# Kernel optimization log

Measured on AMD Instinct MI355X. Metric: run time of the kernel, lower is better.

Reference implementation:

```python
import jax, jax.numpy as jnp
import numpy as np

N_CLASSES = 2
LAMBD = 0.5
BATCH = 16777216  # 2**24


def _cost_matrix(n):
    # M[i, j] = (j - i)**2 for j > i, else 0 (upper-triangular squared distance)
    i = jnp.arange(n)[:, None]
    j = jnp.arange(n)[None, :]
    return jnp.where(j > i, (j - i).astype(jnp.float32) ** 2, 0.0)


def setup_inputs() -> dict:
    key = jax.random.key(0)
    k1, k2 = jax.random.split(key)
    outputs = jax.random.normal(k1, (BATCH, N_CLASSES), dtype=jnp.float32)
    labels = jax.random.randint(k2, (BATCH,), 0, N_CLASSES, dtype=jnp.int64)
    return {"outputs": outputs, "labels": labels}


def reference(outputs, labels):
    n = N_CLASSES
    M = _cost_matrix(n)

    # criterion: cross-entropy with mean reduction
    logp = jax.nn.log_softmax(outputs, axis=-1)           # [B, C]
    ce = -jnp.mean(jnp.take_along_axis(logp, labels[:, None], axis=1))

    # prediction = argmax over classes (torch.max(outputs, 1)[1])
    prediction = jnp.argmax(outputs, axis=1)              # [B]

    # CS = M[prediction, labels] : gather of cost weights
    CS = M[prediction, labels]                            # [B]

    # confusion matrix via single scatter-add histogram: cm[t, p] += 1
    flat_idx = labels * n + prediction
    cm = jax.ops.segment_sum(jnp.ones_like(flat_idx, dtype=jnp.float32),
                             flat_idx, num_segments=n * n)
    TP = cm[1 * n + 1]
    TN = cm[0 * n + 0]
    FP = cm[0 * n + 1]
    FN = cm[1 * n + 0]

    nonzero = (TP > 0) & (TN > 0) & (FP > 0) & (FN > 0)
    # safe ratio (denominators guarded; branch only used when all counts > 0)
    ratio = (TP / jnp.maximum(TP + FN, 1.0)) * (FP / jnp.maximum(FP + TN, 1.0))
    coeff = jnp.where(nonzero,
                      -LAMBD * jnp.log(jnp.sqrt(jnp.maximum(ratio, 1e-30))),
                      LAMBD)

    loss = ce + coeff * jnp.mean(CS)
    return loss
```

## Files before the change

kernel.cpp:

```cpp
#include <hip/hip_runtime.h>
#include <math.h>

#define TPB 256
#define CHUNKS_PER_BLOCK (TPB * 4)
#define TPB_F 1024

typedef float fx4 __attribute__((ext_vector_type(4)));
typedef int   ix4 __attribute__((ext_vector_type(4)));


__device__ __forceinline__ void proc(float o0, float o1, int l,
                                     float& ce, unsigned long long& cnt) {
    const float d = o0 - o1;
    ce += fmaxf(l ? d : -d, 0.0f) + __logf(1.0f + __expf(-fabsf(d)));
    cnt += 1ull << ((((l << 1) | (d < 0.0f ? 1 : 0))) << 4);
}

__global__ __launch_bounds__(TPB) void detloss_main(
    const fx4* __restrict__ out4,
    const ix4* __restrict__ lab4,
    double* __restrict__ ce_part,
    unsigned long long* __restrict__ cnt_part,
    int nchunks)
{
    float ce = 0.0f;
    unsigned long long cnt = 0ull;
    const int tid = threadIdx.x;
    const int g0 = blockIdx.x * CHUNKS_PER_BLOCK + tid;
    const int g1 = g0 + TPB, g2 = g1 + TPB, g3 = g2 + TPB;

    if (g3 < nchunks) {
        const ix4 lb0 = __builtin_nontemporal_load(lab4 + g0);
        const ix4 lb1 = __builtin_nontemporal_load(lab4 + g1);
        const ix4 lb2 = __builtin_nontemporal_load(lab4 + g2);
        const ix4 lb3 = __builtin_nontemporal_load(lab4 + g3);
        const fx4 a0 = __builtin_nontemporal_load(out4 + 2*g0);
        const fx4 b0 = __builtin_nontemporal_load(out4 + 2*g0 + 1);
        const fx4 a1 = __builtin_nontemporal_load(out4 + 2*g1);
        const fx4 b1 = __builtin_nontemporal_load(out4 + 2*g1 + 1);
        const fx4 a2 = __builtin_nontemporal_load(out4 + 2*g2);
        const fx4 b2 = __builtin_nontemporal_load(out4 + 2*g2 + 1);
        const fx4 a3 = __builtin_nontemporal_load(out4 + 2*g3);
        const fx4 b3 = __builtin_nontemporal_load(out4 + 2*g3 + 1);

        proc(a0.x,a0.y,lb0.x,ce,cnt); proc(a0.z,a0.w,lb0.y,ce,cnt);
        proc(b0.x,b0.y,lb0.z,ce,cnt); proc(b0.z,b0.w,lb0.w,ce,cnt);
        proc(a1.x,a1.y,lb1.x,ce,cnt); proc(a1.z,a1.w,lb1.y,ce,cnt);
        proc(b1.x,b1.y,lb1.z,ce,cnt); proc(b1.z,b1.w,lb1.w,ce,cnt);
        proc(a2.x,a2.y,lb2.x,ce,cnt); proc(a2.z,a2.w,lb2.y,ce,cnt);
        proc(b2.x,b2.y,lb2.z,ce,cnt); proc(b2.z,b2.w,lb2.w,ce,cnt);
        proc(a3.x,a3.y,lb3.x,ce,cnt); proc(a3.z,a3.w,lb3.y,ce,cnt);
        proc(b3.x,b3.y,lb3.z,ce,cnt); proc(b3.z,b3.w,lb3.w,ce,cnt);
    } else {
        #pragma unroll
        for (int k = 0; k < 4; ++k) {
            const int g = g0 + k * TPB;
            if (g < nchunks) {
                const ix4 lb = lab4[g];
                const fx4 a = out4[2*g], b = out4[2*g+1];
                proc(a.x,a.y,lb.x,ce,cnt); proc(a.z,a.w,lb.y,ce,cnt);
                proc(b.x,b.y,lb.z,ce,cnt); proc(b.z,b.w,lb.w,ce,cnt);
            }
        }
    }

    #pragma unroll
    for (int off = 32; off > 0; off >>= 1) {
        ce  += __shfl_down(ce, off);
        cnt += __shfl_down(cnt, off);
    }

    __shared__ float              s_ce[TPB / 64];
    __shared__ unsigned long long s_cnt[TPB / 64];
    const int wave = tid >> 6;
    const int lane = tid & 63;
    if (lane == 0) { s_ce[wave] = ce; s_cnt[wave] = cnt; }
    __syncthreads();

    if (tid == 0) {
        float bce = 0.0f;
        unsigned long long bc = 0ull;
        #pragma unroll
        for (int w = 0; w < TPB / 64; ++w) { bce += s_ce[w]; bc += s_cnt[w]; }
        ce_part[blockIdx.x]  = (double)bce;
        cnt_part[blockIdx.x] = bc;
    }
}

__global__ __launch_bounds__(TPB_F) void detloss_final(
    const double* __restrict__ ce_part,
    const unsigned long long* __restrict__ cnt_part,
    float* __restrict__ out, int B, int nparts)
{
    double ce = 0.0;
    unsigned int q0 = 0, q1 = 0, q2 = 0, q3 = 0;
    for (int s = threadIdx.x; s < nparts; s += TPB_F) {
        ce += ce_part[s];
        const unsigned long long c = cnt_part[s];
        q0 += (unsigned int)( c        & 0xffffull);
        q1 += (unsigned int)((c >> 16) & 0xffffull);
        q2 += (unsigned int)((c >> 32) & 0xffffull);
        q3 += (unsigned int)( c >> 48);
    }

    #pragma unroll
    for (int off = 32; off > 0; off >>= 1) {
        ce += __shfl_down(ce, off);
        q0 += __shfl_down(q0, off);
        q1 += __shfl_down(q1, off);
        q2 += __shfl_down(q2, off);
        q3 += __shfl_down(q3, off);
    }

    __shared__ double       s_ce[TPB_F / 64];
    __shared__ unsigned int s_q[4][TPB_F / 64];
    const int wave = threadIdx.x >> 6;
    const int lane = threadIdx.x & 63;
    if (lane == 0) {
        s_ce[wave] = ce;
        s_q[0][wave] = q0; s_q[1][wave] = q1; s_q[2][wave] = q2; s_q[3][wave] = q3;
    }
    __syncthreads();

    if (threadIdx.x == 0) {
        double ceT = 0.0;
        unsigned int TNu = 0, FPu = 0, FNu = 0, TPu = 0;
        #pragma unroll
        for (int w = 0; w < TPB_F / 64; ++w) {
            ceT += s_ce[w];
            TNu += s_q[0][w]; FPu += s_q[1][w]; FNu += s_q[2][w]; TPu += s_q[3][w];
        }
        const double TN = (double)TNu, FP = (double)FPu,
                     FN = (double)FNu, TP = (double)TPu;
        const double invB = 1.0 / (double)B;
        const bool nonzero = (TP > 0.0) && (TN > 0.0) && (FP > 0.0) && (FN > 0.0);
        const double ratio = (TP / fmax(TP + FN, 1.0)) * (FP / fmax(FP + TN, 1.0));
        const double coeff = nonzero ? (-0.5 * log(sqrt(fmax(ratio, 1e-30)))) : 0.5;
        out[0] = (float)(ceT * invB + coeff * FN * invB);
    }
}

extern "C" void kernel_launch(void* const* d_in, const int* in_sizes, int n_in,
                              void* d_out, int out_size, void* d_ws, size_t ws_size,
                              hipStream_t stream) {
    const float* outputs = (const float*)d_in[0];
    const int*   labels  = (const int*)d_in[1];
    const int B = in_sizes[1];

    const int nchunks = B / 4;
    const int nparts  = (nchunks + CHUNKS_PER_BLOCK - 1) / CHUNKS_PER_BLOCK;

    double*             ce_part  = (double*)d_ws;
    unsigned long long* cnt_part = (unsigned long long*)((char*)d_ws
                                                         + (size_t)nparts * sizeof(double));

    detloss_main<<<nparts, TPB, 0, stream>>>(
        (const fx4*)outputs, (const ix4*)labels, ce_part, cnt_part, nchunks);
    detloss_final<<<1, TPB_F, 0, stream>>>(ce_part, cnt_part, (float*)d_out, B, nparts);
}
```

Baseline: 217.0 us.

## Fuse final reduction into main kernel via last-block atomic ticket

```diff
diff --git a/kernel.cpp b/kernel.cpp
--- a/kernel.cpp
+++ b/kernel.cpp
@@ -3,7 +3,6 @@
 
 #define TPB 256
 #define CHUNKS_PER_BLOCK (TPB * 4)
-#define TPB_F 1024
 
 typedef float fx4 __attribute__((ext_vector_type(4)));
 typedef int   ix4 __attribute__((ext_vector_type(4)));
@@ -16,12 +15,14 @@
     cnt += 1ull << ((((l << 1) | (d < 0.0f ? 1 : 0))) << 4);
 }
 
-__global__ __launch_bounds__(TPB) void detloss_main(
+__global__ __launch_bounds__(TPB) void detloss_fused(
     const fx4* __restrict__ out4,
     const ix4* __restrict__ lab4,
-    double* __restrict__ ce_part,
+    unsigned int* __restrict__ ticket,
+    unsigned long long* __restrict__ ce_part,
     unsigned long long* __restrict__ cnt_part,
-    int nchunks)
+    float* __restrict__ out,
+    int B, int nchunks, int nparts)
 {
     float ce = 0.0f;
     unsigned long long cnt = 0ull;
@@ -72,6 +73,7 @@
 
     __shared__ float              s_ce[TPB / 64];
     __shared__ unsigned long long s_cnt[TPB / 64];
+    __shared__ int                s_last;
     const int wave = tid >> 6;
     const int lane = tid & 63;
     if (lane == 0) { s_ce[wave] = ce; s_cnt[wave] = cnt; }
@@ -82,21 +84,26 @@
         unsigned long long bc = 0ull;
         #pragma unroll
         for (int w = 0; w < TPB / 64; ++w) { bce += s_ce[w]; bc += s_cnt[w]; }
-        ce_part[blockIdx.x]  = (double)bce;
-        cnt_part[blockIdx.x] = bc;
+        __hip_atomic_store(&ce_part[blockIdx.x],
+                           (unsigned long long)__double_as_longlong((double)bce),
+                           __ATOMIC_RELEASE, __HIP_MEMORY_SCOPE_AGENT);
+        __hip_atomic_store(&cnt_part[blockIdx.x], bc,
+                           __ATOMIC_RELEASE, __HIP_MEMORY_SCOPE_AGENT);
+        const unsigned int old = __hip_atomic_fetch_add(ticket, 1u,
+                           __ATOMIC_ACQ_REL, __HIP_MEMORY_SCOPE_AGENT);
+        s_last = (old == (unsigned int)(nparts - 1));
     }
-}
+    __syncthreads();
+    if (!s_last) return;
 
-__global__ __launch_bounds__(TPB_F) void detloss_final(
-    const double* __restrict__ ce_part,
-    const unsigned long long* __restrict__ cnt_part,
-    float* __restrict__ out, int B, int nparts)
-{
-    double ce = 0.0;
+    double ced = 0.0;
     unsigned int q0 = 0, q1 = 0, q2 = 0, q3 = 0;
-    for (int s = threadIdx.x; s < nparts; s += TPB_F) {
-        ce += ce_part[s];
-        const unsigned long long c = cnt_part[s];
+    for (int s = tid; s < nparts; s += TPB) {
+        const unsigned long long cb = __hip_atomic_load(&ce_part[s],
+                               __ATOMIC_RELAXED, __HIP_MEMORY_SCOPE_AGENT);
+        ced += __longlong_as_double((long long)cb);
+        const unsigned long long c  = __hip_atomic_load(&cnt_part[s],
+                               __ATOMIC_RELAXED, __HIP_MEMORY_SCOPE_AGENT);
         q0 += (unsigned int)( c        & 0xffffull);
         q1 += (unsigned int)((c >> 16) & 0xffffull);
         q2 += (unsigned int)((c >> 32) & 0xffffull);
@@ -105,30 +112,28 @@
 
     #pragma unroll
     for (int off = 32; off > 0; off >>= 1) {
-        ce += __shfl_down(ce, off);
-        q0 += __shfl_down(q0, off);
-        q1 += __shfl_down(q1, off);
-        q2 += __shfl_down(q2, off);
-        q3 += __shfl_down(q3, off);
+        ced += __shfl_down(ced, off);
+        q0  += __shfl_down(q0, off);
+        q1  += __shfl_down(q1, off);
+        q2  += __shfl_down(q2, off);
+        q3  += __shfl_down(q3, off);
     }
 
-    __shared__ double       s_ce[TPB_F / 64];
-    __shared__ unsigned int s_q[4][TPB_F / 64];
-    const int wave = threadIdx.x >> 6;
-    const int lane = threadIdx.x & 63;
+    __shared__ double       f_ce[TPB / 64];
+    __shared__ unsigned int f_q[4][TPB / 64];
     if (lane == 0) {
-        s_ce[wave] = ce;
-        s_q[0][wave] = q0; s_q[1][wave] = q1; s_q[2][wave] = q2; s_q[3][wave] = q3;
+        f_ce[wave] = ced;
+        f_q[0][wave] = q0; f_q[1][wave] = q1; f_q[2][wave] = q2; f_q[3][wave] = q3;
     }
     __syncthreads();
 
-    if (threadIdx.x == 0) {
+    if (tid == 0) {
         double ceT = 0.0;
         unsigned int TNu = 0, FPu = 0, FNu = 0, TPu = 0;
         #pragma unroll
-        for (int w = 0; w < TPB_F / 64; ++w) {
-            ceT += s_ce[w];
-            TNu += s_q[0][w]; FPu += s_q[1][w]; FNu += s_q[2][w]; TPu += s_q[3][w];
+        for (int w = 0; w < TPB / 64; ++w) {
+            ceT += f_ce[w];
+            TNu += f_q[0][w]; FPu += f_q[1][w]; FNu += f_q[2][w]; TPu += f_q[3][w];
         }
         const double TN = (double)TNu, FP = (double)FPu,
                      FN = (double)FNu, TP = (double)TPu;
@@ -150,11 +155,13 @@
     const int nchunks = B / 4;
     const int nparts  = (nchunks + CHUNKS_PER_BLOCK - 1) / CHUNKS_PER_BLOCK;
 
-    double*             ce_part  = (double*)d_ws;
-    unsigned long long* cnt_part = (unsigned long long*)((char*)d_ws
-                                                         + (size_t)nparts * sizeof(double));
+    unsigned int*       ticket   = (unsigned int*)d_ws;
+    unsigned long long* ce_part  = (unsigned long long*)((char*)d_ws + 256);
+    unsigned long long* cnt_part = ce_part + nparts;
 
-    detloss_main<<<nparts, TPB, 0, stream>>>(
-        (const fx4*)outputs, (const ix4*)labels, ce_part, cnt_part, nchunks);
-    detloss_final<<<1, TPB_F, 0, stream>>>(ce_part, cnt_part, (float*)d_out, B, nparts);
+    hipMemsetAsync(d_ws, 0, 64, stream);
+
+    detloss_fused<<<nparts, TPB, 0, stream>>>(
+        (const fx4*)outputs, (const ix4*)labels,
+        ticket, ce_part, cnt_part, (float*)d_out, B, nchunks, nparts);
 }
```

Result: slower. 719.9 us (+231.8%).
